# Kernel optimization log

Hardware: AMD Instinct MI355X
Metric: run time of the kernel (lower is better)

The kernel has to match this reference:

```python
import jax, jax.numpy as jnp
import numpy as np

N = 100000
E = 800000
D_IN = 256
D_H = 512


def setup_inputs() -> dict:
    key = jax.random.key(0)
    ks = jax.random.split(key, 8)
    s_in = 1.0 / np.sqrt(D_IN)
    s_h = 1.0 / np.sqrt(D_H)
    return {
        "x": jax.random.normal(ks[0], (N, D_IN), jnp.float32),
        "edge_index": jax.random.randint(ks[1], (2, E), 0, N, dtype=jnp.int64),
        "W1": jax.random.normal(ks[2], (D_IN, D_H), jnp.float32) * s_in,
        "b1": jnp.zeros((D_H,), jnp.float32),
        "W2": jax.random.normal(ks[3], (D_H, D_H), jnp.float32) * s_h,
        "b2": jnp.zeros((D_H,), jnp.float32),
        "W3": jax.random.normal(ks[4], (D_H, D_H), jnp.float32) * s_h,
        "b3": jnp.zeros((D_H,), jnp.float32),
        "Wfc": jax.random.normal(ks[5], (D_H, D_IN), jnp.float32) * s_h,
        "bfc": jnp.zeros((D_IN,), jnp.float32),
    }


def _gcn_prep(edge_index, n_nodes):
    # PyG GCNConv: add self-loops, symmetric deg^{-1/2} normalization.
    loop = jnp.arange(n_nodes, dtype=edge_index.dtype)
    row = jnp.concatenate([edge_index[0], loop])  # destination
    col = jnp.concatenate([edge_index[1], loop])  # source
    deg = jax.ops.segment_sum(jnp.ones_like(row, dtype=jnp.float32), row,
                              num_segments=n_nodes)
    dinv = jax.lax.rsqrt(deg)  # deg >= 1 due to self loops
    norm = dinv[row] * dinv[col]  # [E+N]
    return row, col, norm


def _gcn_conv(x, W, b, row, col, norm, n_nodes):
    h = x @ W  # [N, out]
    msg = h[col] * norm[:, None]  # [E+N, out] gather + scale
    out = jax.ops.segment_sum(msg, row, num_segments=n_nodes)  # scatter-add
    return out + b


def reference(x, edge_index, W1, b1, W2, b2, W3, b3, Wfc, bfc):
    n = x.shape[0]
    row, col, norm = _gcn_prep(edge_index, n)
    h = jax.nn.relu(_gcn_conv(x, W1, b1, row, col, norm, n))
    h = jax.nn.relu(_gcn_conv(h, W2, b2, row, col, norm, n))
    h = jax.nn.relu(_gcn_conv(h, W3, b3, row, col, norm, n))
    return h @ Wfc + bfc
```

## Files before the change

kernel.cpp:

```cpp
#include <hip/hip_runtime.h>

#define N_NODES 100000
#define NPAD    100096
#define E_EDGES 800000

typedef _Float16 f16;
typedef _Float16 f16x4 __attribute__((ext_vector_type(4)));
typedef _Float16 f16x8 __attribute__((ext_vector_type(8)));
typedef float    f32x4 __attribute__((ext_vector_type(4)));

__device__ inline void async16(const void* g, void* l) {
    __builtin_amdgcn_global_load_lds(
        (const __attribute__((address_space(1))) void*)g,
        (__attribute__((address_space(3))) void*)l, 16, 0, 0);
}

__global__ void k_deg(const int* __restrict__ ei, int* __restrict__ deg) {
    int e = blockIdx.x * 256 + threadIdx.x;
    if (e < E_EDGES) atomicAdd(&deg[ei[e]], 1);
}

__global__ void k_dinv(const int* __restrict__ deg, float* __restrict__ dinv) {
    int i = blockIdx.x * 256 + threadIdx.x;
    if (i < N_NODES) dinv[i] = rsqrtf((float)(deg[i] + 1));
}

__global__ void k_scan1(const int* __restrict__ deg, int* __restrict__ off,
                        int* __restrict__ bsum) {
    __shared__ int s[256];
    int i = blockIdx.x * 256 + threadIdx.x;
    int v = (i < N_NODES) ? deg[i] : 0;
    s[threadIdx.x] = v;
    __syncthreads();
    for (int d = 1; d < 256; d <<= 1) {
        int t = (threadIdx.x >= d) ? s[threadIdx.x - d] : 0;
        __syncthreads();
        s[threadIdx.x] += t;
        __syncthreads();
    }
    if (i < N_NODES) off[i] = s[threadIdx.x] - v;
    if (threadIdx.x == 255) bsum[blockIdx.x] = s[255];
}

__global__ void k_scan2(int* __restrict__ bsum, int nb) {
    __shared__ int s[512];
    int tid = threadIdx.x;
    int v = (tid < nb) ? bsum[tid] : 0;
    s[tid] = v;
    __syncthreads();
    for (int d = 1; d < 512; d <<= 1) {
        int t = (tid >= d) ? s[tid - d] : 0;
        __syncthreads();
        s[tid] += t;
        __syncthreads();
    }
    if (tid < nb) bsum[tid] = s[tid] - v;
}

__global__ void k_scan3(int* __restrict__ off, const int* __restrict__ bsum) {
    int i = blockIdx.x * 256 + threadIdx.x;
    if (i < N_NODES) off[i] += bsum[blockIdx.x];
    if (i == 0) off[N_NODES] = E_EDGES;
}

__global__ void k_fill(const int* __restrict__ ei, const int* __restrict__ off,
                       int* __restrict__ cursor, int* __restrict__ csr) {
    int e = blockIdx.x * 256 + threadIdx.x;
    if (e >= E_EDGES) return;
    int dst = ei[e];
    int src = ei[E_EDGES + e];
    int pos = atomicAdd(&cursor[dst], 1);
    csr[off[dst] + pos] = src;
}

__global__ void k_x_to_f16(const float* __restrict__ x, f16* __restrict__ xh) {
    int i = blockIdx.x * 256 + threadIdx.x;
    if (i >= (N_NODES * 256) / 4) return;
    float4 v = ((const float4*)x)[i];
    f16x4 o;
    o.x = (f16)v.x; o.y = (f16)v.y; o.z = (f16)v.z; o.w = (f16)v.w;
    ((f16x4*)xh)[i] = o;
}

__global__ void k_transpose(const float* __restrict__ W, f16* __restrict__ Wt,
                            int K, int M) {
    int m = blockIdx.x * 256 + threadIdx.x;
    int k = blockIdx.y;
    if (m < M) Wt[(size_t)m * K + k] = (f16)W[(size_t)k * M + m];
}

template<int K, int M, bool FINAL>
__launch_bounds__(256, 2)
__global__ void k_gemm(const f16* __restrict__ A, const f16* __restrict__ B,
                       void* __restrict__ C, const float* __restrict__ bias) {
    __shared__ f16 As[128 * 32];
    __shared__ f16 Bs[128 * 32];
    int tid  = threadIdx.x;
    int wave = tid >> 6, lane = tid & 63;
    int wr = (wave >> 1) * 64, wc = (wave & 1) * 64;
    int lm = lane & 15, q = lane >> 4;
    int rowBase = blockIdx.x * 128;
    int colBase = blockIdx.y * 128;

    f32x4 acc[4][4] = {};
    const f16* Ag = A + (size_t)rowBase * K;
    const f16* Bg = B + (size_t)colBase * K;

    int c0 = tid, c1 = tid + 256;
    for (int kt = 0; kt < K; kt += 32) {
        __syncthreads();
        async16(Ag + (size_t)(c0 >> 2) * K + kt + (c0 & 3) * 8, &As[c0 * 8]);
        async16(Ag + (size_t)(c1 >> 2) * K + kt + (c1 & 3) * 8, &As[c1 * 8]);
        async16(Bg + (size_t)(c0 >> 2) * K + kt + (c0 & 3) * 8, &Bs[c0 * 8]);
        async16(Bg + (size_t)(c1 >> 2) * K + kt + (c1 & 3) * 8, &Bs[c1 * 8]);
        __syncthreads();

        f16x8 a[4], b[4];
#pragma unroll
        for (int i = 0; i < 4; ++i) {
            a[i] = *(const f16x8*)&As[(wr + i * 16 + lm) * 32 + q * 8];
            b[i] = *(const f16x8*)&Bs[(wc + i * 16 + lm) * 32 + q * 8];
        }
#pragma unroll
        for (int i = 0; i < 4; ++i)
#pragma unroll
            for (int j = 0; j < 4; ++j)
                acc[i][j] = __builtin_amdgcn_mfma_f32_16x16x32_f16(
                    a[i], b[j], acc[i][j], 0, 0, 0);
    }

#pragma unroll
    for (int i = 0; i < 4; ++i) {
        int gr0 = rowBase + wr + i * 16 + q * 4;
#pragma unroll
        for (int j = 0; j < 4; ++j) {
            int gc = colBase + wc + j * 16 + lm;
#pragma unroll
            for (int r = 0; r < 4; ++r) {
                int gr = gr0 + r;
                if (gr < N_NODES) {
                    float v = acc[i][j][r];
                    if (FINAL)
                        ((float*)C)[(size_t)gr * M + gc] = v + bias[gc];
                    else
                        ((f16*)C)[(size_t)gr * M + gc] = (f16)v;
                }
            }
        }
    }
}

__global__ void k_agg(const f16* __restrict__ t, const int* __restrict__ off,
                      const int* __restrict__ csr, const float* __restrict__ dinv,
                      const float* __restrict__ bias, f16* __restrict__ h) {
    int node = blockIdx.x * 4 + (threadIdx.x >> 6);
    if (node >= N_NODES) return;
    int lane = threadIdx.x & 63;
    float di = dinv[node];

    f16x8 v = ((const f16x8*)(t + (size_t)node * 512))[lane];
    float acc[8];
#pragma unroll
    for (int j = 0; j < 8; ++j) acc[j] = di * (float)v[j];

    int s = off[node], e = off[node + 1];
    for (int idx = s; idx < e; ++idx) {
        int src = csr[idx];
        float dj = dinv[src];
        f16x8 u = ((const f16x8*)(t + (size_t)src * 512))[lane];
#pragma unroll
        for (int j = 0; j < 8; ++j) acc[j] += dj * (float)u[j];
    }

    const float* bl = bias + lane * 8;
    f16x8 o;
#pragma unroll
    for (int j = 0; j < 8; ++j) {
        float r = di * acc[j] + bl[j];
        o[j] = (f16)(r > 0.f ? r : 0.f);
    }
    ((f16x8*)(h + (size_t)node * 512))[lane] = o;
}

extern "C" void kernel_launch(void* const* d_in, const int* in_sizes, int n_in,
                              void* d_out, int out_size, void* d_ws, size_t ws_size,
                              hipStream_t stream) {
    const float* x   = (const float*)d_in[0];
    const int*   ei  = (const int*)d_in[1];
    const float* W1  = (const float*)d_in[2];
    const float* b1  = (const float*)d_in[3];
    const float* W2  = (const float*)d_in[4];
    const float* b2  = (const float*)d_in[5];
    const float* W3  = (const float*)d_in[6];
    const float* b3  = (const float*)d_in[7];
    const float* Wfc = (const float*)d_in[8];
    const float* bfc = (const float*)d_in[9];

    char* wsb = (char*)d_ws;
    size_t o = 0;
    auto alloc = [&](size_t bytes) -> void* {
        void* p = wsb + o;
        o += (bytes + 255) & ~(size_t)255;
        return p;
    };

    f16* xh   = (f16*)alloc((size_t)NPAD * 256 * 2);
    f16* t    = (f16*)alloc((size_t)NPAD * 512 * 2);
    f16* h    = (f16*)alloc((size_t)NPAD * 512 * 2);
    f16* Wt1  = (f16*)alloc(512 * 256 * 2);
    f16* Wt2  = (f16*)alloc(512 * 512 * 2);
    f16* Wt3  = (f16*)alloc(512 * 512 * 2);
    f16* Wtfc = (f16*)alloc(256 * 512 * 2);
    int* deg    = (int*)alloc(N_NODES * 4);
    float* dinv = (float*)alloc(N_NODES * 4);
    int* off    = (int*)alloc((N_NODES + 1) * 4);
    int* cursor = (int*)alloc(N_NODES * 4);
    int* bsum   = (int*)alloc(4096 * 4);
    int* csr    = (int*)alloc((size_t)E_EDGES * 4);

    const int NB = (N_NODES + 255) / 256;

    hipMemsetAsync(deg, 0, N_NODES * 4, stream);
    hipMemsetAsync(cursor, 0, N_NODES * 4, stream);

    k_deg<<<(E_EDGES + 255) / 256, 256, 0, stream>>>(ei, deg);
    k_dinv<<<NB, 256, 0, stream>>>(deg, dinv);
    k_scan1<<<NB, 256, 0, stream>>>(deg, off, bsum);
    k_scan2<<<1, 512, 0, stream>>>(bsum, NB);
    k_scan3<<<NB, 256, 0, stream>>>(off, bsum);
    k_fill<<<(E_EDGES + 255) / 256, 256, 0, stream>>>(ei, off, cursor, csr);

    k_x_to_f16<<<(N_NODES * 256 / 4 + 255) / 256, 256, 0, stream>>>(x, xh);
    k_transpose<<<dim3(2, 256), 256, 0, stream>>>(W1, Wt1, 256, 512);
    k_transpose<<<dim3(2, 512), 256, 0, stream>>>(W2, Wt2, 512, 512);
    k_transpose<<<dim3(2, 512), 256, 0, stream>>>(W3, Wt3, 512, 512);
    k_transpose<<<dim3(1, 512), 256, 0, stream>>>(Wfc, Wtfc, 512, 256);

    dim3 g4(NPAD / 128, 4), g2(NPAD / 128, 2);

    k_gemm<256, 512, false><<<g4, 256, 0, stream>>>(xh, Wt1, t, nullptr);
    k_agg<<<N_NODES / 4, 256, 0, stream>>>(t, off, csr, dinv, b1, h);
    k_gemm<512, 512, false><<<g4, 256, 0, stream>>>(h, Wt2, t, nullptr);
    k_agg<<<N_NODES / 4, 256, 0, stream>>>(t, off, csr, dinv, b2, h);
    k_gemm<512, 512, false><<<g4, 256, 0, stream>>>(h, Wt3, t, nullptr);
    k_agg<<<N_NODES / 4, 256, 0, stream>>>(t, off, csr, dinv, b3, h);
    k_gemm<512, 256, true><<<g2, 256, 0, stream>>>(h, Wtfc, d_out, bfc);
}
```

Before: 995.1 us.

## Aggregate before first GEMM on narrow features, fuse bias-ReLU, unroll gathers

Layer 1 now aggregates the 256-wide input features first and then multiplies by W1 (A·X·W instead of A·(X·W)). This halves the gather traffic for that layer, and bias plus ReLU move into the GEMM epilogue. The aggregation kernel is templated on width, and its neighbor loop is unrolled by 4 so more independent row loads are in flight. The dinv computation is folded into the first scan kernel, which removes one launch. Reordering the product changes where fp16 rounding happens.

```diff
diff --git a/kernel.cpp b/kernel.cpp
--- a/kernel.cpp
+++ b/kernel.cpp
@@ -20,16 +20,12 @@
     if (e < E_EDGES) atomicAdd(&deg[ei[e]], 1);
 }
 
-__global__ void k_dinv(const int* __restrict__ deg, float* __restrict__ dinv) {
-    int i = blockIdx.x * 256 + threadIdx.x;
-    if (i < N_NODES) dinv[i] = rsqrtf((float)(deg[i] + 1));
-}
-
 __global__ void k_scan1(const int* __restrict__ deg, int* __restrict__ off,
-                        int* __restrict__ bsum) {
+                        int* __restrict__ bsum, float* __restrict__ dinv) {
     __shared__ int s[256];
     int i = blockIdx.x * 256 + threadIdx.x;
     int v = (i < N_NODES) ? deg[i] : 0;
+    if (i < N_NODES) dinv[i] = rsqrtf((float)(v + 1));
     s[threadIdx.x] = v;
     __syncthreads();
     for (int d = 1; d < 256; d <<= 1) {
@@ -89,7 +85,7 @@
     if (m < M) Wt[(size_t)m * K + k] = (f16)W[(size_t)k * M + m];
 }
 
-template<int K, int M, bool FINAL>
+template<int K, int M, int MODE>
 __launch_bounds__(256, 2)
 __global__ void k_gemm(const f16* __restrict__ A, const f16* __restrict__ B,
                        void* __restrict__ C, const float* __restrict__ bias) {
@@ -140,46 +136,74 @@
                 int gr = gr0 + r;
                 if (gr < N_NODES) {
                     float v = acc[i][j][r];
-                    if (FINAL)
+                    if (MODE == 2) {
                         ((float*)C)[(size_t)gr * M + gc] = v + bias[gc];
-                    else
+                    } else if (MODE == 1) {
+                        float rr = v + bias[gc];
+                        ((f16*)C)[(size_t)gr * M + gc] = (f16)(rr > 0.f ? rr : 0.f);
+                    } else {
                         ((f16*)C)[(size_t)gr * M + gc] = (f16)v;
+                    }
                 }
             }
         }
     }
 }
 
+template<int VE> struct VecT;
+template<> struct VecT<4> { typedef f16x4 type; };
+template<> struct VecT<8> { typedef f16x8 type; };
+
+template<int CH, bool ACT>
 __global__ void k_agg(const f16* __restrict__ t, const int* __restrict__ off,
                       const int* __restrict__ csr, const float* __restrict__ dinv,
                       const float* __restrict__ bias, f16* __restrict__ h) {
+    constexpr int VE = CH / 64;
+    typedef typename VecT<VE>::type vec;
     int node = blockIdx.x * 4 + (threadIdx.x >> 6);
     if (node >= N_NODES) return;
     int lane = threadIdx.x & 63;
     float di = dinv[node];
 
-    f16x8 v = ((const f16x8*)(t + (size_t)node * 512))[lane];
-    float acc[8];
-#pragma unroll
-    for (int j = 0; j < 8; ++j) acc[j] = di * (float)v[j];
+    const vec* rows = (const vec*)t;
+    vec v = rows[(size_t)node * 64 + lane];
+    float acc[VE];
+#pragma unroll
+    for (int j = 0; j < VE; ++j) acc[j] = di * (float)v[j];
 
     int s = off[node], e = off[node + 1];
-    for (int idx = s; idx < e; ++idx) {
+    int idx = s;
+    for (; idx + 4 <= e; idx += 4) {
+        int i0 = csr[idx], i1 = csr[idx + 1], i2 = csr[idx + 2], i3 = csr[idx + 3];
+        vec u0 = rows[(size_t)i0 * 64 + lane];
+        vec u1 = rows[(size_t)i1 * 64 + lane];
+        vec u2 = rows[(size_t)i2 * 64 + lane];
+        vec u3 = rows[(size_t)i3 * 64 + lane];
+        float d0 = dinv[i0], d1 = dinv[i1], d2 = dinv[i2], d3 = dinv[i3];
+#pragma unroll
+        for (int j = 0; j < VE; ++j)
+            acc[j] += d0 * (float)u0[j] + d1 * (float)u1[j]
+                    + d2 * (float)u2[j] + d3 * (float)u3[j];
+    }
+    for (; idx < e; ++idx) {
         int src = csr[idx];
         float dj = dinv[src];
-        f16x8 u = ((const f16x8*)(t + (size_t)src * 512))[lane];
-#pragma unroll
-        for (int j = 0; j < 8; ++j) acc[j] += dj * (float)u[j];
-    }
-
-    const float* bl = bias + lane * 8;
-    f16x8 o;
-#pragma unroll
-    for (int j = 0; j < 8; ++j) {
-        float r = di * acc[j] + bl[j];
-        o[j] = (f16)(r > 0.f ? r : 0.f);
-    }
-    ((f16x8*)(h + (size_t)node * 512))[lane] = o;
+        vec u = rows[(size_t)src * 64 + lane];
+#pragma unroll
+        for (int j = 0; j < VE; ++j) acc[j] += dj * (float)u[j];
+    }
+
+    vec o;
+#pragma unroll
+    for (int j = 0; j < VE; ++j) {
+        float r = di * acc[j];
+        if (ACT) {
+            r += bias[lane * VE + j];
+            r = r > 0.f ? r : 0.f;
+        }
+        o[j] = (f16)r;
+    }
+    ((vec*)h)[(size_t)node * 64 + lane] = o;
 }
 
 extern "C" void kernel_launch(void* const* d_in, const int* in_sizes, int n_in,
@@ -218,14 +242,15 @@
     int* bsum   = (int*)alloc(4096 * 4);
     int* csr    = (int*)alloc((size_t)E_EDGES * 4);
 
+    f16* a1 = t;
+
     const int NB = (N_NODES + 255) / 256;
 
     hipMemsetAsync(deg, 0, N_NODES * 4, stream);
     hipMemsetAsync(cursor, 0, N_NODES * 4, stream);
 
     k_deg<<<(E_EDGES + 255) / 256, 256, 0, stream>>>(ei, deg);
-    k_dinv<<<NB, 256, 0, stream>>>(deg, dinv);
-    k_scan1<<<NB, 256, 0, stream>>>(deg, off, bsum);
+    k_scan1<<<NB, 256, 0, stream>>>(deg, off, bsum, dinv);
     k_scan2<<<1, 512, 0, stream>>>(bsum, NB);
     k_scan3<<<NB, 256, 0, stream>>>(off, bsum);
     k_fill<<<(E_EDGES + 255) / 256, 256, 0, stream>>>(ei, off, cursor, csr);
@@ -237,12 +262,13 @@
     k_transpose<<<dim3(1, 512), 256, 0, stream>>>(Wfc, Wtfc, 512, 256);
 
     dim3 g4(NPAD / 128, 4), g2(NPAD / 128, 2);
-
-    k_gemm<256, 512, false><<<g4, 256, 0, stream>>>(xh, Wt1, t, nullptr);
-    k_agg<<<N_NODES / 4, 256, 0, stream>>>(t, off, csr, dinv, b1, h);
-    k_gemm<512, 512, false><<<g4, 256, 0, stream>>>(h, Wt2, t, nullptr);
-    k_agg<<<N_NODES / 4, 256, 0, stream>>>(t, off, csr, dinv, b2, h);
-    k_gemm<512, 512, false><<<g4, 256, 0, stream>>>(h, Wt3, t, nullptr);
-    k_agg<<<N_NODES / 4, 256, 0, stream>>>(t, off, csr, dinv, b3, h);
-    k_gemm<512, 256, true><<<g2, 256, 0, stream>>>(h, Wtfc, d_out, bfc);
-}
+    const int AGG_GRID = N_NODES / 4;
+
+    k_agg<256, false><<<AGG_GRID, 256, 0, stream>>>(xh, off, csr, dinv, nullptr, a1);
+    k_gemm<256, 512, 1><<<g4, 256, 0, stream>>>(a1, Wt1, h, b1);
+    k_gemm<512, 512, 0><<<g4, 256, 0, stream>>>(h, Wt2, t, nullptr);
+    k_agg<512, true><<<AGG_GRID, 256, 0, stream>>>(t, off, csr, dinv, b2, h);
+    k_gemm<512, 512, 0><<<g4, 256, 0, stream>>>(h, Wt3, t, nullptr);
+    k_agg<512, true><<<AGG_GRID, 256, 0, stream>>>(t, off, csr, dinv, b3, h);
+    k_gemm<512, 256, 2><<<g2, 256, 0, stream>>>(h, Wtfc, d_out, bfc);
+}
```

Result: faster. 942.5 us (-5.3%).
